# Kernel optimization log

Measured on AMD Instinct MI355X. Metric: run time of the kernel, lower is better.

## Reference

```python
import jax, jax.numpy as jnp
import numpy as np

B, T, D = 2, 2048, 2048
H, HD, RD = 16, 192, 64
CD = HD - RD          # 128 content dims per head
QR, DL = 768, 512     # q lora rank, kv latent dim
THETA = 10000.0


def setup_inputs() -> dict:
    key = jax.random.key(0)
    ks = jax.random.split(key, 9)
    s = 0.02
    return {
        "x": jax.random.normal(ks[0], (B, T, D), jnp.float32),
        "wq_down": jax.random.normal(ks[1], (D, QR), jnp.float32) * s,
        "wq_up": jax.random.normal(ks[2], (QR, H * CD), jnp.float32) * s,
        "wq_rope": jax.random.normal(ks[3], (D, H * RD), jnp.float32) * s,
        "wkv_down": jax.random.normal(ks[4], (D, DL), jnp.float32) * s,
        "wk_up": jax.random.normal(ks[5], (DL, H * CD), jnp.float32) * s,
        "wv_up": jax.random.normal(ks[6], (DL, H * HD), jnp.float32) * s,
        "wk_rope": jax.random.normal(ks[7], (D, H * RD), jnp.float32) * s,
        "wo": jax.random.normal(ks[8], (H * HD, D), jnp.float32) * s,
    }


def _rope_tables(seq_len):
    inv = 1.0 / (THETA ** (jnp.arange(0, RD, 2, dtype=jnp.float32) / RD))  # [RD/2]
    ang = jnp.arange(seq_len, dtype=jnp.float32)[:, None] * inv[None, :]  # [T, RD/2]
    return jnp.cos(ang), jnp.sin(ang)


def _apply_rope(x, cos, sin):
    # x: [B,H,T,RD]; cos/sin: [T,RD/2] broadcast over B,H
    d = RD // 2
    x1, x2 = x[..., :d], x[..., d:]
    return jnp.concatenate([x1 * cos - x2 * sin, x1 * sin + x2 * cos], axis=-1)


def reference(x, wq_down, wq_up, wq_rope, wkv_down, wk_up, wv_up, wk_rope, wo):
    # projections
    q_c = (x @ wq_down) @ wq_up                       # [B,T,H*CD]
    q_p = x @ wq_rope                                 # [B,T,H*RD]
    latent = x @ wkv_down                             # [B,T,DL]
    k_c = latent @ wk_up                              # [B,T,H*CD]
    k_p = x @ wk_rope                                 # [B,T,H*RD]
    v = latent @ wv_up                                # [B,T,H*HD]

    def heads(t, d):
        return t.reshape(B, T, H, d).transpose(0, 2, 1, 3)  # [B,H,T,d]

    q_c, q_p = heads(q_c, CD), heads(q_p, RD)
    k_c, k_p = heads(k_c, CD), heads(k_p, RD)
    v = heads(v, HD)

    cos, sin = _rope_tables(T)
    q_p = _apply_rope(q_p, cos, sin)
    k_p = _apply_rope(k_p, cos, sin)

    q = jnp.concatenate([q_c, q_p], axis=-1)          # [B,H,T,HD]
    k = jnp.concatenate([k_c, k_p], axis=-1)          # [B,H,T,HD]

    scale = 1.0 / jnp.sqrt(jnp.asarray(HD, q.dtype))
    scores = jnp.einsum("bhqd,bhkd->bhqk", q, k) * scale
    causal = jnp.tril(jnp.ones((T, T), dtype=bool))
    scores = jnp.where(causal, scores, jnp.finfo(scores.dtype).min)
    attn = jax.nn.softmax(scores, axis=-1)
    out = jnp.einsum("bhqk,bhkd->bhqd", attn, v)      # [B,H,T,HD]
    out = out.transpose(0, 2, 1, 3).reshape(B, T, H * HD)
    return out @ wo                                   # [B,T,D]
```

## Files before the change

### kernel.cpp

```cpp
#include <hip/hip_runtime.h>
#include <hip/hip_bf16.h>
#include <cstdint>
#include <cstddef>

typedef __bf16 bf16_t;
typedef __bf16 bf16x8 __attribute__((ext_vector_type(8)));
typedef float f32x4 __attribute__((ext_vector_type(4)));

#define MFMA16(a, b, c) __builtin_amdgcn_mfma_f32_16x16x32_bf16((a), (b), (c), 0, 0, 0)

__device__ __forceinline__ void gload_lds16(const void* g, void* l) {
  __builtin_amdgcn_global_load_lds((__attribute__((address_space(1))) void*)(g),
                                   (__attribute__((address_space(3))) void*)(l),
                                   16, 0, 0);
}

__device__ __forceinline__ uint32_t pkbf(float lo, float hi) {
  union { bf16_t h[2]; uint32_t u; } u2;
  u2.h[0] = (bf16_t)lo; u2.h[1] = (bf16_t)hi;
  return u2.u;
}

__global__ __launch_bounds__(256) void cvt_f32_to_bf16(const float* __restrict__ in,
                                                       bf16_t* __restrict__ out) {
  size_t i = ((size_t)blockIdx.x * 256 + threadIdx.x) * 4;
  float4 v = *(const float4*)(in + i);
  bf16_t o[4] = {(bf16_t)v.x, (bf16_t)v.y, (bf16_t)v.z, (bf16_t)v.w};
  *(uint2*)(out + i) = *(uint2*)o;
}

__global__ __launch_bounds__(256) void transpose_all(
    const float* __restrict__ s0, const float* __restrict__ s1,
    const float* __restrict__ s2, const float* __restrict__ s3,
    const float* __restrict__ s4, const float* __restrict__ s5,
    const float* __restrict__ s6, const float* __restrict__ s7,
    bf16_t* __restrict__ t0, bf16_t* __restrict__ t1, bf16_t* __restrict__ t2,
    bf16_t* __restrict__ t3, bf16_t* __restrict__ t4, bf16_t* __restrict__ t5,
    bf16_t* __restrict__ t6, bf16_t* __restrict__ t7) {
  __shared__ bf16_t tile[32][33];
  const int lid = blockIdx.x;
  const float* src; bf16_t* dst; int R, C, bx, by;
  if (lid < 1536)       { src=s0; dst=t0; R=2048; C=768;  int lo=lid;        bx=lo%24; by=lo/24; }
  else if (lid < 2560)  { src=s1; dst=t1; R=2048; C=512;  int lo=lid-1536;   bx=lo%16; by=lo/16; }
  else if (lid < 4608)  { src=s2; dst=t2; R=2048; C=1024; int lo=lid-2560;   bx=lo%32; by=lo/32; }
  else if (lid < 6656)  { src=s3; dst=t3; R=2048; C=1024; int lo=lid-4608;   bx=lo%32; by=lo/32; }
  else if (lid < 8192)  { src=s4; dst=t4; R=768;  C=2048; int lo=lid-6656;   bx=lo%64; by=lo/64; }
  else if (lid < 9216)  { src=s5; dst=t5; R=512;  C=2048; int lo=lid-8192;   bx=lo%64; by=lo/64; }
  else if (lid < 10752) { src=s6; dst=t6; R=512;  C=3072; int lo=lid-9216;   bx=lo%96; by=lo/96; }
  else                  { src=s7; dst=t7; R=3072; C=2048; int lo=lid-10752;  bx=lo%64; by=lo/64; }
  const int c0 = bx * 32, r0 = by * 32;
  const int tx = threadIdx.x, ty = threadIdx.y;
#pragma unroll
  for (int s = 0; s < 4; s++) {
    int r = ty + s * 8;
    tile[r][tx] = (bf16_t)src[(size_t)(r0 + r) * C + c0 + tx];
  }
  __syncthreads();
#pragma unroll
  for (int s = 0; s < 4; s++) {
    int r = ty + s * 8;
    dst[(size_t)(c0 + r) * R + r0 + tx] = tile[tx][r];
  }
}

__global__ __launch_bounds__(256) void rope_both(bf16_t* __restrict__ qb,
                                                 bf16_t* __restrict__ kb) {
  const int gid = blockIdx.x;
  bf16_t* buf = (gid < 8192) ? qb : kb;
  int idx = (gid & 8191) * 256 + threadIdx.x;
  int j = idx & 31;
  int h = (idx >> 5) & 15;
  int row = idx >> 9;
  int t = row & 2047;
  size_t base = (size_t)row * 3072 + h * 192 + 128;
  float inv = expf(-(float)j * 0.28782313662425574f);
  float ang = (float)t * inv;
  float c, s;
  sincosf(ang, &s, &c);
  float x1 = (float)buf[base + j];
  float x2 = (float)buf[base + j + 32];
  buf[base + j]      = (bf16_t)(x1 * c - x2 * s);
  buf[base + j + 32] = (bf16_t)(x1 * s + x2 * c);
}

template <int MODE>
__global__ __launch_bounds__(512, 4) void gemm128(const bf16_t* __restrict__ A, int lda,
                                                  const bf16_t* __restrict__ Bt,
                                                  void* __restrict__ C0, void* __restrict__ C1,
                                                  void* __restrict__ C2, int K, int ldc) {
  __shared__ __align__(16) bf16_t sA0[128 * 64];
  __shared__ __align__(16) bf16_t sB0[128 * 64];
  __shared__ __align__(16) bf16_t sA1[128 * 64];
  __shared__ __align__(16) bf16_t sB1[128 * 64];
  const int tid = threadIdx.x;
  const int l = tid & 63, w = tid >> 6;
  const int l15 = l & 15, l4 = (l >> 4) & 3;
  const int wr = w >> 1, wc = w & 1;
  const int m0 = blockIdx.y * 128, n0 = blockIdx.x * 128;
  const int nt = K >> 6;

  f32x4 acc[2][4] = {};

#define STAGEG(SA, SB, KT)                                                          \
  {                                                                                 \
    const int kts = (KT) * 64;                                                      \
    _Pragma("unroll")                                                               \
    for (int r = 0; r < 2; r++) {                                                   \
      int i = r * 512 + tid;                                                        \
      int row = i >> 3, cl = i & 7;                                                 \
      int cg = cl ^ (row & 7);                                                      \
      gload_lds16(A + (size_t)(m0 + row) * lda + kts + cg * 8,                      \
                  (char*)(SA) + (size_t)(r * 512 + w * 64) * 16);                   \
    }                                                                               \
    _Pragma("unroll")                                                               \
    for (int r = 0; r < 2; r++) {                                                   \
      int i = r * 512 + tid;                                                        \
      int row = i >> 3, cl = i & 7;                                                 \
      int cg = cl ^ (row & 7);                                                      \
      gload_lds16(Bt + (size_t)(n0 + row) * K + kts + cg * 8,                       \
                  (char*)(SB) + (size_t)(r * 512 + w * 64) * 16);                   \
    }                                                                               \
  }

#define GCOMPUTE(SA, SB)                                                            \
  {                                                                                 \
    _Pragma("unroll")                                                               \
    for (int ks = 0; ks < 2; ks++) {                                                \
      bf16x8 af[2], bfr[4];                                                         \
      _Pragma("unroll")                                                             \
      for (int mf = 0; mf < 2; mf++) {                                              \
        int row = wr * 32 + mf * 16 + l15;                                          \
        int cl = (ks * 4 + l4) ^ (row & 7);                                         \
        af[mf] = *(const bf16x8*)((SA) + row * 64 + cl * 8);                        \
      }                                                                             \
      _Pragma("unroll")                                                             \
      for (int nf = 0; nf < 4; nf++) {                                              \
        int row = wc * 64 + nf * 16 + l15;                                          \
        int cl = (ks * 4 + l4) ^ (row & 7);                                         \
        bfr[nf] = *(const bf16x8*)((SB) + row * 64 + cl * 8);                       \
      }                                                                             \
      __builtin_amdgcn_s_setprio(1);                                                \
      _Pragma("unroll")                                                             \
      for (int mf = 0; mf < 2; mf++)                                                \
        _Pragma("unroll")                                                           \
        for (int nf = 0; nf < 4; nf++)                                              \
          acc[mf][nf] = MFMA16(af[mf], bfr[nf], acc[mf][nf]);                       \
      __builtin_amdgcn_s_setprio(0);                                                \
    }                                                                               \
  }

  STAGEG(sA0, sB0, 0)
  for (int t = 0; t < nt; t += 2) {
    STAGEG(sA1, sB1, t + 1)
    asm volatile("s_waitcnt vmcnt(4)\n\ts_barrier" ::: "memory");
    GCOMPUTE(sA0, sB0)
    asm volatile("s_barrier" ::: "memory");
    if (t + 2 < nt) {
      STAGEG(sA0, sB0, t + 2)
      asm volatile("s_waitcnt vmcnt(4)\n\ts_barrier" ::: "memory");
    } else {
      asm volatile("s_waitcnt vmcnt(0)\n\ts_barrier" ::: "memory");
    }
    GCOMPUTE(sA1, sB1)
    asm volatile("s_barrier" ::: "memory");
  }
#undef STAGEG
#undef GCOMPUTE

#pragma unroll
  for (int mf = 0; mf < 2; mf++)
#pragma unroll
    for (int nf = 0; nf < 4; nf++) {
      const int mbase = m0 + wr * 32 + mf * 16 + l4 * 4;
      const int n = n0 + wc * 64 + nf * 16 + l15;
      if constexpr (MODE == 1) {
#pragma unroll
        for (int r = 0; r < 4; r++)
          ((float*)C0)[(size_t)(mbase + r) * ldc + n] = acc[mf][nf][r];
      } else if constexpr (MODE == 2) {
#pragma unroll
        for (int r = 0; r < 4; r++)
          ((bf16_t*)C0)[(size_t)(mbase + r) * 3072 + (n >> 7) * 192 + (n & 127)] =
              (bf16_t)acc[mf][nf][r];
      } else if constexpr (MODE == 4) {
        if (n < 1280) {
#pragma unroll
          for (int r = 0; r < 4; r++)
            ((bf16_t*)C0)[(size_t)(mbase + r) * 1280 + n] = (bf16_t)acc[mf][nf][r];
        } else if (n < 2304) {
          int nn = n - 1280;
#pragma unroll
          for (int r = 0; r < 4; r++)
            ((bf16_t*)C1)[(size_t)(mbase + r) * 3072 + (nn >> 6) * 192 + 128 + (nn & 63)] =
                (bf16_t)acc[mf][nf][r];
        } else {
          int nn = n - 2304;
#pragma unroll
          for (int r = 0; r < 4; r++)
            ((bf16_t*)C2)[(size_t)(mbase + r) * 3072 + (nn >> 6) * 192 + 128 + (nn & 63)] =
                (bf16_t)acc[mf][nf][r];
        }
      } else {
        if (n < 2048) {
#pragma unroll
          for (int r = 0; r < 4; r++)
            ((bf16_t*)C0)[(size_t)(mbase + r) * 3072 + (n >> 7) * 192 + (n & 127)] =
                (bf16_t)acc[mf][nf][r];
        } else {
          int nn = n - 2048;
          int hh = nn / 192, dd = nn - hh * 192;
          int bb = mbase >> 11, tt = mbase & 2047;
          bf16_t pk4[4] = {(bf16_t)acc[mf][nf][0], (bf16_t)acc[mf][nf][1],
                           (bf16_t)acc[mf][nf][2], (bf16_t)acc[mf][nf][3]};
          *(uint2*)((bf16_t*)C1 + ((size_t)(bb * 16 + hh) * 192 + dd) * 2048 + tt) =
              *(uint2*)pk4;
        }
      }
    }
}

__global__ __launch_bounds__(512, 2) void attn_kernel(const bf16_t* __restrict__ q,
                                                      const bf16_t* __restrict__ kbuf,
                                                      const bf16_t* __restrict__ vt,
                                                      bf16_t* __restrict__ ao) {
  __shared__ __align__(16) bf16_t sK0[64][192];
  __shared__ __align__(16) bf16_t sK1[64][192];
  __shared__ __align__(16) bf16_t sV0[192][64];
  __shared__ __align__(16) bf16_t sV1[192][64];

  const int tid = threadIdx.x, l = tid & 63, w = tid >> 6;
  const int l15 = l & 15, l4 = (l >> 4) & 3;
  const int bh = blockIdx.x & 31;
  const int c = blockIdx.x >> 5;
  const int b = bh >> 4, h = bh & 15;
  const int ca = c, cb = 15 - c;
  const int ra = ca * 128 + w * 16;
  const int rb = cb * 128 + w * 16;
  const int tga = 2 * ca + (w >> 2);
  const int tgb = 2 * cb + (w >> 2);

  const bf16_t* qp = q + (size_t)b * 2048 * 3072 + h * 192;
  const bf16_t* kp = kbuf + (size_t)b * 2048 * 3072 + h * 192;
  const bf16_t* vp = vt + (size_t)bh * 192 * 2048;

  bf16x8 qf[2][6];
#pragma unroll
  for (int kd = 0; kd < 6; kd++) {
    qf[0][kd] = *(const bf16x8*)(qp + (size_t)(ra + l15) * 3072 + kd * 32 + l4 * 8);
    qf[1][kd] = *(const bf16x8*)(qp + (size_t)(rb + l15) * 3072 + kd * 32 + l4 * 8);
  }

  f32x4 o[2][12] = {};
  float mrow[2] = {-__builtin_inff(), -__builtin_inff()};
  float lrow[2] = {0.0f, 0.0f};

  const float scale = 0.07216878364870322f;
  const float THR = 7.0f;
  const int nkt = 2 * cb + 2;
  const int src0 = l15 + ((l4 & 1) << 5);
  const int src1 = src0 + 16;
  const bool hibank = (l4 & 2) != 0;

#define STAGE(SK, SV, KT)                                                           \
  {                                                                                 \
    const int k0s = (KT) * 64;                                                      \
    _Pragma("unroll")                                                               \
    for (int r = 0; r < 3; r++) {                                                   \
      int i = r * 512 + tid;                                                        \
      int row = i / 24, cc = i % 24;                                                \
      int g = cc - (row & 7) * 3;                                                   \
      if (g < 0) g += 24;                                                           \
      gload_lds16(kp + (size_t)(k0s + row) * 3072 + g * 8,                          \
                  (char*)&SK[0][0] + (size_t)(r * 512 + w * 64) * 16);              \
    }                                                                               \
    _Pragma("unroll")                                                               \
    for (int r = 0; r < 3; r++) {                                                   \
      int i = r * 512 + tid;                                                        \
      int d = i >> 3, cc = i & 7;                                                   \
      gload_lds16(vp + (size_t)d * 2048 + k0s + (cc ^ (d & 7)) * 8,                 \
                  (char*)&SV[0][0] + (size_t)(r * 512 + w * 64) * 16);              \
    }                                                                               \
  }

#define SOFTMAX_CHUNK(c, rbase, tg)                                                    \
    {                                                                                  \
      const bool diag = (kt == (tg));                                                  \
      _Pragma("unroll")                                                                \
      for (int nf = 0; nf < 4; nf++)                                                   \
        _Pragma("unroll")                                                              \
        for (int r = 0; r < 4; r++) {                                                  \
          float sv = s[c][nf][r] * scale;                                              \
          if (diag) {                                                                  \
            int ktok = k0 + nf * 16 + l4 * 4 + r;                                      \
            if (ktok > (rbase) + l15) sv = -__builtin_inff();                          \
          }                                                                            \
          s[c][nf][r] = sv;                                                            \
        }                                                                              \
      float m_in = s[c][0][0];                                                         \
      _Pragma("unroll")                                                                \
      for (int nf = 0; nf < 4; nf++)                                                   \
        _Pragma("unroll")                                                              \
        for (int r = 0; r < 4; r++)                                                    \
          if (nf | r) m_in = fmaxf(m_in, s[c][nf][r]);                                 \
      m_in = fmaxf(m_in, __shfl_xor(m_in, 16));                                        \
      m_in = fmaxf(m_in, __shfl_xor(m_in, 32));                                        \
      if (!__all(m_in - mrow[c] <= THR)) {                                             \
        float mn = fmaxf(mrow[c], m_in);                                               \
        float alpha = __expf(mrow[c] - mn);                                            \
        mrow[c] = mn;                                                                  \
        lrow[c] *= alpha;                                                              \
        f32x4 av;                                                                      \
        _Pragma("unroll")                                                              \
        for (int r = 0; r < 4; r++) av[r] = __shfl(alpha, l4 * 4 + r);                 \
        _Pragma("unroll")                                                              \
        for (int nf2 = 0; nf2 < 12; nf2++) o[c][nf2] *= av;                            \
      }                                                                                \
      float rs = 0.0f;                                                                 \
      _Pragma("unroll")                                                                \
      for (int nf = 0; nf < 4; nf++)                                                   \
        _Pragma("unroll")                                                              \
        for (int r = 0; r < 4; r++) {                                                  \
          float pv = __expf(s[c][nf][r] - mrow[c]);                                    \
          s[c][nf][r] = pv;                                                            \
          rs += pv;                                                                    \
        }                                                                              \
      rs += __shfl_xor(rs, 16);                                                        \
      rs += __shfl_xor(rs, 32);                                                        \
      lrow[c] += rs;                                                                   \
      uint32_t wq[8];                                                                  \
      _Pragma("unroll")                                                                \
      for (int nf = 0; nf < 4; nf++) {                                                 \
        wq[nf * 2 + 0] = pkbf(s[c][nf][0], s[c][nf][1]);                               \
        wq[nf * 2 + 1] = pkbf(s[c][nf][2], s[c][nf][3]);                               \
      }                                                                                \
      _Pragma("unroll")                                                                \
      for (int ks = 0; ks < 2; ks++) {                                                 \
        uint32_t A0 = __shfl(wq[(2 * ks) * 2 + 0], src0);                              \
        uint32_t A1 = __shfl(wq[(2 * ks) * 2 + 1], src0);                              \
        uint32_t B0 = __shfl(wq[(2 * ks + 1) * 2 + 0], src0);                          \
        uint32_t B1 = __shfl(wq[(2 * ks + 1) * 2 + 1], src0);                          \
        uint32_t C0w = __shfl(wq[(2 * ks) * 2 + 0], src1);                             \
        uint32_t C1w = __shfl(wq[(2 * ks) * 2 + 1], src1);                             \
        uint32_t D0 = __shfl(wq[(2 * ks + 1) * 2 + 0], src1);                          \
        uint32_t D1 = __shfl(wq[(2 * ks + 1) * 2 + 1], src1);                          \
        union { uint32_t u[4]; bf16x8 v; } fr;                                         \
        fr.u[0] = hibank ? B0 : A0;                                                    \
        fr.u[1] = hibank ? B1 : A1;                                                    \
        fr.u[2] = hibank ? D0 : C0w;                                                   \
        fr.u[3] = hibank ? D1 : C1w;                                                   \
        pa[c][ks] = fr.v;                                                              \
      }                                                                                \
    }

#define TILE_BODY(SK, SV, KT)                                                          \
  {                                                                                    \
    const int kt = (KT);                                                               \
    const int k0 = kt * 64;                                                            \
    const bool act_a = (kt <= tga);                                                    \
    const bool act_b = (kt <= tgb);                                                    \
    f32x4 s[2][4] = {};                                                                \
    __builtin_amdgcn_s_setprio(1);                                                     \
    _Pragma("unroll")                                                                  \
    for (int kd = 0; kd < 6; kd++) {                                                   \
      bf16x8 bk[4];                                                                    \
      _Pragma("unroll")                                                                \
      for (int nf = 0; nf < 4; nf++) {                                                 \
        int row = nf * 16 + l15;                                                       \
        int cl = kd * 4 + l4 + (row & 7) * 3;                                          \
        if (cl >= 24) cl -= 24;                                                        \
        bk[nf] = *(const bf16x8*)(&SK[row][cl * 8]);                                   \
      }                                                                                \
      if (act_b) {                                                                     \
        _Pragma("unroll")                                                              \
        for (int nf = 0; nf < 4; nf++)                                                 \
          s[1][nf] = MFMA16(bk[nf], qf[1][kd], s[1][nf]);                              \
      }                                                                                \
      if (act_a) {                                                                     \
        _Pragma("unroll")                                                              \
        for (int nf = 0; nf < 4; nf++)                                                 \
          s[0][nf] = MFMA16(bk[nf], qf[0][kd], s[0][nf]);                              \
      }                                                                                \
    }                                                                                  \
    __builtin_amdgcn_s_setprio(0);                                                     \
    bf16x8 pa[2][2] = {};                                                              \
    if (act_b) SOFTMAX_CHUNK(1, rb, tgb)                                               \
    if (act_a) SOFTMAX_CHUNK(0, ra, tga)                                               \
    __builtin_amdgcn_s_setprio(1);                                                     \
    _Pragma("unroll")                                                                  \
    for (int ks = 0; ks < 2; ks++) {                                                   \
      _Pragma("unroll")                                                                \
      for (int nf2 = 0; nf2 < 12; nf2++) {                                             \
        int d = nf2 * 16 + l15;                                                        \
        int cl = (ks * 4 + l4) ^ (d & 7);                                              \
        bf16x8 vb = *(const bf16x8*)(&SV[d][cl * 8]);                                  \
        if (act_b) o[1][nf2] = MFMA16(pa[1][ks], vb, o[1][nf2]);                       \
        if (act_a) o[0][nf2] = MFMA16(pa[0][ks], vb, o[0][nf2]);                       \
      }                                                                                \
    }                                                                                  \
    __builtin_amdgcn_s_setprio(0);                                                     \
  }

  STAGE(sK0, sV0, 0)
  __syncthreads();

  for (int kt0 = 0; kt0 < nkt; kt0 += 2) {
    STAGE(sK1, sV1, kt0 + 1)
    TILE_BODY(sK0, sV0, kt0)
    __syncthreads();
    if (kt0 + 2 < nkt) STAGE(sK0, sV0, kt0 + 2)
    TILE_BODY(sK1, sV1, kt0 + 1)
    __syncthreads();
  }
#undef STAGE
#undef SOFTMAX_CHUNK
#undef TILE_BODY

#pragma unroll
  for (int mf = 0; mf < 2; mf++) {
    const int rbase = (mf == 0) ? ra : rb;
#pragma unroll
    for (int r = 0; r < 4; r++) {
      float lv = __shfl(lrow[mf], l4 * 4 + r);
      float inv = 1.0f / lv;
      int qrow = rbase + l4 * 4 + r;
#pragma unroll
      for (int nf2 = 0; nf2 < 12; nf2++) {
        int d = nf2 * 16 + l15;
        ao[(size_t)(b * 2048 + qrow) * 3072 + h * 192 + d] = (bf16_t)(o[mf][nf2][r] * inv);
      }
    }
  }
}

extern "C" void kernel_launch(void* const* d_in, const int* in_sizes, int n_in,
                              void* d_out, int out_size, void* d_ws, size_t ws_size,
                              hipStream_t stream) {
  const float* x       = (const float*)d_in[0];
  const float* wq_down = (const float*)d_in[1];
  const float* wq_up   = (const float*)d_in[2];
  const float* wq_rope = (const float*)d_in[3];
  const float* wkv_down= (const float*)d_in[4];
  const float* wk_up   = (const float*)d_in[5];
  const float* wv_up   = (const float*)d_in[6];
  const float* wk_rope = (const float*)d_in[7];
  const float* wo      = (const float*)d_in[8];
  float* out = (float*)d_out;

  char* p = (char*)d_ws;
  auto take = [&](size_t elems) { bf16_t* r = (bf16_t*)p; p += elems * 2; return r; };
  bf16_t* xb    = take(4096ull * 2048);
  bf16_t* fw1   = take(3328ull * 2048);
  bf16_t* wqu_t = take(2048ull * 768);
  bf16_t* fw2   = take(5120ull * 512);
  bf16_t* wo_t  = take(2048ull * 3072);
  bf16_t* qkvd  = take(4096ull * 1280);
  bf16_t* qbuf  = take(4096ull * 3072);
  bf16_t* kbuf  = take(4096ull * 3072);
  bf16_t* ao    = take(4096ull * 3072);
  bf16_t* vt    = take(4096ull * 3072);

  dim3 tb(32, 8);
  cvt_f32_to_bf16<<<8192, 256, 0, stream>>>(x, xb);
  transpose_all<<<16896, tb, 0, stream>>>(
      wq_down, wkv_down, wq_rope, wk_rope, wq_up, wk_up, wv_up, wo,
      fw1, fw1 + 768ull * 2048, fw1 + 1280ull * 2048, fw1 + 2304ull * 2048,
      wqu_t, fw2, fw2 + 2048ull * 512, wo_t);

  gemm128<4><<<dim3(26, 32), 512, 0, stream>>>(xb, 2048, fw1, qkvd, qbuf, kbuf, 2048, 0);
  gemm128<2><<<dim3(16, 32), 512, 0, stream>>>(qkvd, 1280, wqu_t, qbuf, nullptr, nullptr, 768, 0);
  gemm128<5><<<dim3(40, 32), 512, 0, stream>>>(qkvd + 768, 1280, fw2, kbuf, vt, nullptr, 512, 0);

  rope_both<<<16384, 256, 0, stream>>>(qbuf, kbuf);

  attn_kernel<<<256, 512, 0, stream>>>(qbuf, kbuf, vt, ao);

  gemm128<1><<<dim3(16, 32), 512, 0, stream>>>(ao, 3072, wo_t, out, nullptr, nullptr, 3072, 2048);
}
```

Baseline: 326.4 us.

## Fuse RoPE into projection GEMM epilogue and load V directly from global

Result: slower. 643.6 us (+97.2%).

```diff
diff --git a/kernel.cpp b/kernel.cpp
--- a/kernel.cpp
+++ b/kernel.cpp
@@ -61,26 +61,6 @@
     int r = ty + s * 8;
     dst[(size_t)(c0 + r) * R + r0 + tx] = tile[tx][r];
   }
-}
-
-__global__ __launch_bounds__(256) void rope_both(bf16_t* __restrict__ qb,
-                                                 bf16_t* __restrict__ kb) {
-  const int gid = blockIdx.x;
-  bf16_t* buf = (gid < 8192) ? qb : kb;
-  int idx = (gid & 8191) * 256 + threadIdx.x;
-  int j = idx & 31;
-  int h = (idx >> 5) & 15;
-  int row = idx >> 9;
-  int t = row & 2047;
-  size_t base = (size_t)row * 3072 + h * 192 + 128;
-  float inv = expf(-(float)j * 0.28782313662425574f);
-  float ang = (float)t * inv;
-  float c, s;
-  sincosf(ang, &s, &c);
-  float x1 = (float)buf[base + j];
-  float x2 = (float)buf[base + j + 32];
-  buf[base + j]      = (bf16_t)(x1 * c - x2 * s);
-  buf[base + j + 32] = (bf16_t)(x1 * s + x2 * c);
 }
 
 template <int MODE>
@@ -167,6 +147,29 @@
 #undef STAGEG
 #undef GCOMPUTE
 
+  if constexpr (MODE == 4) {
+    if (n0 + wc * 64 >= 1280) {
+      float inv0 = expf(-(float)l15 * 0.28782313662425574f);
+      float inv1 = expf(-(float)(l15 + 16) * 0.28782313662425574f);
+#pragma unroll
+      for (int mf = 0; mf < 2; mf++)
+#pragma unroll
+        for (int r = 0; r < 4; r++) {
+          int m = m0 + wr * 32 + mf * 16 + l4 * 4 + r;
+          float tt = (float)(m & 2047);
+          float c0v, s0v, c1v, s1v;
+          sincosf(tt * inv0, &s0v, &c0v);
+          sincosf(tt * inv1, &s1v, &c1v);
+          float x1a = acc[mf][0][r], x2a = acc[mf][2][r];
+          acc[mf][0][r] = x1a * c0v - x2a * s0v;
+          acc[mf][2][r] = x1a * s0v + x2a * c0v;
+          float x1b = acc[mf][1][r], x2b = acc[mf][3][r];
+          acc[mf][1][r] = x1b * c1v - x2b * s1v;
+          acc[mf][3][r] = x1b * s1v + x2b * c1v;
+        }
+    }
+  }
+
 #pragma unroll
   for (int mf = 0; mf < 2; mf++)
 #pragma unroll
@@ -225,8 +228,6 @@
                                                       bf16_t* __restrict__ ao) {
   __shared__ __align__(16) bf16_t sK0[64][192];
   __shared__ __align__(16) bf16_t sK1[64][192];
-  __shared__ __align__(16) bf16_t sV0[192][64];
-  __shared__ __align__(16) bf16_t sV1[192][64];
 
   const int tid = threadIdx.x, l = tid & 63, w = tid >> 6;
   const int l15 = l & 15, l4 = (l >> 4) & 3;
@@ -261,7 +262,7 @@
   const int src1 = src0 + 16;
   const bool hibank = (l4 & 2) != 0;
 
-#define STAGE(SK, SV, KT)                                                           \
+#define STAGE(SK, KT)                                                               \
   {                                                                                 \
     const int k0s = (KT) * 64;                                                      \
     _Pragma("unroll")                                                               \
@@ -272,13 +273,6 @@
       if (g < 0) g += 24;                                                           \
       gload_lds16(kp + (size_t)(k0s + row) * 3072 + g * 8,                          \
                   (char*)&SK[0][0] + (size_t)(r * 512 + w * 64) * 16);              \
-    }                                                                               \
-    _Pragma("unroll")                                                               \
-    for (int r = 0; r < 3; r++) {                                                   \
-      int i = r * 512 + tid;                                                        \
-      int d = i >> 3, cc = i & 7;                                                   \
-      gload_lds16(vp + (size_t)d * 2048 + k0s + (cc ^ (d & 7)) * 8,                 \
-                  (char*)&SV[0][0] + (size_t)(r * 512 + w * 64) * 16);              \
     }                                                                               \
   }
 
@@ -352,12 +346,19 @@
       }                                                                                \
     }
 
-#define TILE_BODY(SK, SV, KT)                                                          \
+#define TILE_BODY(SK, KT)                                                              \
   {                                                                                    \
     const int kt = (KT);                                                               \
     const int k0 = kt * 64;                                                            \
     const bool act_a = (kt <= tga);                                                    \
     const bool act_b = (kt <= tgb);                                                    \
+    uint4 vb0[12], vb1[12];                                                            \
+    _Pragma("unroll")                                                                  \
+    for (int nf2 = 0; nf2 < 12; nf2++) {                                               \
+      int d = nf2 * 16 + l15;                                                          \
+      vb0[nf2] = *(const uint4*)(vp + (size_t)d * 2048 + k0 + l4 * 8);                 \
+    }                                                                                  \
+    __builtin_amdgcn_sched_barrier(0);                                                 \
     f32x4 s[2][4] = {};                                                                \
     __builtin_amdgcn_s_setprio(1);                                                     \
     _Pragma("unroll")                                                                  \
@@ -382,33 +383,40 @@
       }                                                                                \
     }                                                                                  \
     __builtin_amdgcn_s_setprio(0);                                                     \
+    _Pragma("unroll")                                                                  \
+    for (int nf2 = 0; nf2 < 12; nf2++) {                                               \
+      int d = nf2 * 16 + l15;                                                          \
+      vb1[nf2] = *(const uint4*)(vp + (size_t)d * 2048 + k0 + 32 + l4 * 8);            \
+    }                                                                                  \
+    __builtin_amdgcn_sched_barrier(0);                                                 \
     bf16x8 pa[2][2] = {};                                                              \
     if (act_b) SOFTMAX_CHUNK(1, rb, tgb)                                               \
     if (act_a) SOFTMAX_CHUNK(0, ra, tga)                                               \
     __builtin_amdgcn_s_setprio(1);                                                     \
     _Pragma("unroll")                                                                  \
-    for (int ks = 0; ks < 2; ks++) {                                                   \
-      _Pragma("unroll")                                                                \
-      for (int nf2 = 0; nf2 < 12; nf2++) {                                             \
-        int d = nf2 * 16 + l15;                                                        \
-        int cl = (ks * 4 + l4) ^ (d & 7);                                              \
-        bf16x8 vb = *(const bf16x8*)(&SV[d][cl * 8]);                                  \
-        if (act_b) o[1][nf2] = MFMA16(pa[1][ks], vb, o[1][nf2]);                       \
-        if (act_a) o[0][nf2] = MFMA16(pa[0][ks], vb, o[0][nf2]);                       \
-      }                                                                                \
+    for (int nf2 = 0; nf2 < 12; nf2++) {                                               \
+      bf16x8 vb = *(const bf16x8*)&vb0[nf2];                                           \
+      if (act_b) o[1][nf2] = MFMA16(pa[1][0], vb, o[1][nf2]);                          \
+      if (act_a) o[0][nf2] = MFMA16(pa[0][0], vb, o[0][nf2]);                          \
+    }                                                                                  \
+    _Pragma("unroll")                                                                  \
+    for (int nf2 = 0; nf2 < 12; nf2++) {                                               \
+      bf16x8 vb = *(const bf16x8*)&vb1[nf2];                                           \
+      if (act_b) o[1][nf2] = MFMA16(pa[1][1], vb, o[1][nf2]);                          \
+      if (act_a) o[0][nf2] = MFMA16(pa[0][1], vb, o[0][nf2]);                          \
     }                                                                                  \
     __builtin_amdgcn_s_setprio(0);                                                     \
   }
 
-  STAGE(sK0, sV0, 0)
+  STAGE(sK0, 0)
   __syncthreads();
 
   for (int kt0 = 0; kt0 < nkt; kt0 += 2) {
-    STAGE(sK1, sV1, kt0 + 1)
-    TILE_BODY(sK0, sV0, kt0)
+    STAGE(sK1, kt0 + 1)
+    TILE_BODY(sK0, kt0)
     __syncthreads();
-    if (kt0 + 2 < nkt) STAGE(sK0, sV0, kt0 + 2)
-    TILE_BODY(sK1, sV1, kt0 + 1)
+    if (kt0 + 2 < nkt) STAGE(sK0, kt0 + 2)
+    TILE_BODY(sK1, kt0 + 1)
     __syncthreads();
   }
 #undef STAGE
@@ -470,8 +478,6 @@
   gemm128<2><<<dim3(16, 32), 512, 0, stream>>>(qkvd, 1280, wqu_t, qbuf, nullptr, nullptr, 768, 0);
   gemm128<5><<<dim3(40, 32), 512, 0, stream>>>(qkvd + 768, 1280, fw2, kbuf, vt, nullptr, 512, 0);
 
-  rope_both<<<16384, 256, 0, stream>>>(qbuf, kbuf);
-
   attn_kernel<<<256, 512, 0, stream>>>(qbuf, kbuf, vt, ao);
 
   gemm128<1><<<dim3(16, 32), 512, 0, stream>>>(ao, 3072, wo_t, out, nullptr, nullptr, 3072, 2048);
```
